# Optimization experiments

Measured on AMD Instinct MI355X. Metric: run time of the kernel, lower is better.

The kernel has to match this reference:

```python
import jax, jax.numpy as jnp
import numpy as np

T, H, F, E, K = 4096, 1024, 4096, 8, 2


def setup_inputs() -> dict:
    key = jax.random.key(0)
    ks = jax.random.split(key, 6)
    hidden_states = jax.random.normal(ks[0], (T, H), dtype=jnp.float32)
    expert_weights = jax.random.uniform(ks[1], (T, K), dtype=jnp.float32)
    selected_experts = jax.random.randint(ks[2], (T, K), 0, E, dtype=jnp.int64)
    W1 = 0.02 * jax.random.normal(ks[3], (E, H, F), dtype=jnp.float32)
    b1 = jnp.zeros((E, F), dtype=jnp.float32)
    W2 = 0.02 * jax.random.normal(ks[4], (E, F, H), dtype=jnp.float32)
    b2 = jnp.zeros((E, H), dtype=jnp.float32)
    return {"hidden_states": hidden_states, "expert_weights": expert_weights,
            "W1": W1, "b1": b1, "W2": W2, "b2": b2,
            "selected_experts": selected_experts}


def reference(hidden_states, expert_weights, W1, b1, W2, b2, selected_experts):
    # Combine weight per (token, expert): sum of routing weights over top-k
    # slots assigned to that expert; slots with expert_idx < 0 contribute 0.
    num_experts = W1.shape[0]
    onehot = (selected_experts[:, :, None] == jnp.arange(num_experts)[None, None, :])
    valid = (selected_experts >= 0)[:, :, None]
    cw = jnp.einsum('tk,tke->te', expert_weights,
                    (onehot & valid).astype(hidden_states.dtype))  # [T, E]

    out = jnp.zeros_like(hidden_states)
    for e in range(num_experts):  # small fixed expert count
        h = jax.nn.gelu(hidden_states @ W1[e] + b1[e], approximate=False)  # [T, F]
        y = h @ W2[e] + b2[e]                                              # [T, H]
        out = out + cw[:, e:e + 1] * y
    return out
```

## Files before the change

### kernel.cpp

```cpp
#include <hip/hip_runtime.h>
#include <hip/hip_bf16.h>

#define Td 4096
#define Hd 1024
#define Fd 4096
#define Ed 8
#define Rcap 8704

typedef __attribute__((ext_vector_type(8))) short bf16x8;
typedef __attribute__((ext_vector_type(4))) float f32x4;
typedef __attribute__((ext_vector_type(8))) unsigned short u16x8;

__device__ __forceinline__ unsigned short f32_to_bf16(float x) {
  unsigned int u = __float_as_uint(x);
  unsigned int r = (u + 0x7FFFu + ((u >> 16) & 1u)) >> 16;
  return (unsigned short)r;
}

__global__ __launch_bounds__(256) void cvt_bf16_kernel(const float* __restrict__ in,
                                                       unsigned short* __restrict__ outp, int n8) {
  int i = blockIdx.x * 256 + threadIdx.x;
  if (i >= n8) return;
  const float4* p = (const float4*)(in + (size_t)i * 8);
  float4 a = p[0], b = p[1];
  u16x8 o;
  o[0] = f32_to_bf16(a.x); o[1] = f32_to_bf16(a.y); o[2] = f32_to_bf16(a.z); o[3] = f32_to_bf16(a.w);
  o[4] = f32_to_bf16(b.x); o[5] = f32_to_bf16(b.y); o[6] = f32_to_bf16(b.z); o[7] = f32_to_bf16(b.w);
  *(u16x8*)(outp + (size_t)i * 8) = o;
}

__global__ __launch_bounds__(256) void transpose_cvt_kernel(const float* __restrict__ in,
                                                            unsigned short* __restrict__ outp,
                                                            int Rdm, int Cdm) {
  __shared__ float tile[64][68];
  int tilesR = Rdm >> 6, tilesC = Cdm >> 6;
  int per = tilesR * tilesC;
  int bid = blockIdx.x;
  int e = bid / per; int rem = bid - e * per;
  int tr = rem / tilesC; int tc = rem - tr * tilesC;
  int r0 = tr << 6, c0 = tc << 6;
  int tid = threadIdx.x;
  int rr = tid >> 2, cq = (tid & 3) << 4;
  const float* src = in + ((size_t)e * Rdm + r0 + rr) * Cdm + c0 + cq;
  float4 v0 = ((const float4*)src)[0];
  float4 v1 = ((const float4*)src)[1];
  float4 v2 = ((const float4*)src)[2];
  float4 v3 = ((const float4*)src)[3];
  *(float4*)&tile[rr][cq + 0]  = v0;
  *(float4*)&tile[rr][cq + 4]  = v1;
  *(float4*)&tile[rr][cq + 8]  = v2;
  *(float4*)&tile[rr][cq + 12] = v3;
  __syncthreads();
  u16x8 o0, o1;
#pragma unroll
  for (int j = 0; j < 8; j++) o0[j] = f32_to_bf16(tile[cq + j][rr]);
#pragma unroll
  for (int j = 0; j < 8; j++) o1[j] = f32_to_bf16(tile[cq + 8 + j][rr]);
  unsigned short* dst = outp + ((size_t)e * Cdm + c0 + rr) * Rdm + r0 + cq;
  *(u16x8*)dst = o0;
  *(u16x8*)(dst + 8) = o1;
}

__global__ void init_meta_kernel(int* cnt) {
  if (threadIdx.x < Ed) cnt[threadIdx.x] = 0;
}

__global__ __launch_bounds__(256) void route_kernel(const int* __restrict__ sel,
                                                    const float* __restrict__ ew,
                                                    int* cnt, int* idxT, float* wgtT) {
  int t = blockIdx.x * 256 + threadIdx.x;
  if (t >= Td) return;
  int e0 = sel[t * 2], e1 = sel[t * 2 + 1];
  float w0 = ew[t * 2], w1 = ew[t * 2 + 1];
  if (e0 == e1) { w0 += w1; e1 = -1; }
  if (e0 >= 0 && e0 < Ed) { int p = atomicAdd(&cnt[e0], 1); idxT[e0 * Td + p] = t; wgtT[e0 * Td + p] = w0; }
  if (e1 >= 0 && e1 < Ed) { int p = atomicAdd(&cnt[e1], 1); idxT[e1 * Td + p] = t; wgtT[e1 * Td + p] = w1; }
}

__global__ void scan_kernel(const int* cnt, int* off) {
  if (threadIdx.x == 0) {
    int acc = 0; off[0] = 0;
#pragma unroll
    for (int e = 0; e < Ed; e++) { acc += (cnt[e] + 63) & ~63; off[e + 1] = acc; }
  }
}

__global__ __launch_bounds__(256) void compact_kernel(const int* __restrict__ cnt,
                                                      const int* __restrict__ off,
                                                      const int* __restrict__ idxT,
                                                      const float* __restrict__ wgtT,
                                                      int* __restrict__ cidx,
                                                      float* __restrict__ cwgt) {
  int j = blockIdx.x * 256 + threadIdx.x;
  int e = j >> 12; int i = j & (Td - 1);
  int base = off[e], end = off[e + 1];
  int row = base + i;
  if (row < end) {
    if (i < cnt[e]) { cidx[row] = idxT[e * Td + i]; cwgt[row] = wgtT[e * Td + i]; }
    else            { cidx[row] = -1;               cwgt[row] = 0.f; }
  }
}

template <bool FIRST, int KD, int NC>
__global__ __launch_bounds__(256) void gemm_kernel(const unsigned short* __restrict__ Abase,
                                                   const unsigned short* __restrict__ Bt,
                                                   const float* __restrict__ bias,
                                                   const int* __restrict__ cidx,
                                                   const float* __restrict__ cwgt,
                                                   const int* __restrict__ off,
                                                   unsigned short* __restrict__ hbuf,
                                                   float* __restrict__ outp) {
  int row0 = blockIdx.y << 6;
  int tot = off[Ed];
  if (row0 >= tot) return;
  int e = 0;
  while (off[e + 1] <= row0) ++e;
  int n0 = blockIdx.x << 6;

  __shared__ unsigned short As[64][72];
  __shared__ unsigned short Bs[64][72];

  const int tid = threadIdx.x;
  const int sr = tid >> 2, sk = (tid & 3) << 4;

  bool avalid = true;
  const unsigned short* aptr;
  if (FIRST) {
    int t = cidx[row0 + sr];
    avalid = (t >= 0);
    aptr = Abase + (size_t)(avalid ? t : 0) * KD + sk;
  } else {
    aptr = Abase + (size_t)(row0 + sr) * KD + sk;
  }
  const unsigned short* bptr = Bt + ((size_t)e * NC + n0 + sr) * KD + sk;

  const int lane = tid & 63, wid = tid >> 6;
  const int wr = wid >> 1, wc = wid & 1;
  const int fr = lane & 15, fk = (lane >> 4) << 3;

  f32x4 acc[2][2] = {};

  for (int k0 = 0; k0 < KD; k0 += 64) {
    uint4 a0v = make_uint4(0, 0, 0, 0), a1v = a0v;
    if (avalid) {
      a0v = ((const uint4*)(aptr + k0))[0];
      a1v = ((const uint4*)(aptr + k0))[1];
    }
    uint4 b0v = ((const uint4*)(bptr + k0))[0];
    uint4 b1v = ((const uint4*)(bptr + k0))[1];
    __syncthreads();
    *(uint4*)(&As[sr][sk])     = a0v;
    *(uint4*)(&As[sr][sk + 8]) = a1v;
    *(uint4*)(&Bs[sr][sk])     = b0v;
    *(uint4*)(&Bs[sr][sk + 8]) = b1v;
    __syncthreads();
#pragma unroll
    for (int ks = 0; ks < 64; ks += 32) {
      bf16x8 af0 = *(const bf16x8*)(&As[(wr << 5) + fr][ks + fk]);
      bf16x8 af1 = *(const bf16x8*)(&As[(wr << 5) + 16 + fr][ks + fk]);
      bf16x8 bg0 = *(const bf16x8*)(&Bs[(wc << 5) + fr][ks + fk]);
      bf16x8 bg1 = *(const bf16x8*)(&Bs[(wc << 5) + 16 + fr][ks + fk]);
      acc[0][0] = __builtin_amdgcn_mfma_f32_16x16x32_bf16(af0, bg0, acc[0][0], 0, 0, 0);
      acc[0][1] = __builtin_amdgcn_mfma_f32_16x16x32_bf16(af0, bg1, acc[0][1], 0, 0, 0);
      acc[1][0] = __builtin_amdgcn_mfma_f32_16x16x32_bf16(af1, bg0, acc[1][0], 0, 0, 0);
      acc[1][1] = __builtin_amdgcn_mfma_f32_16x16x32_bf16(af1, bg1, acc[1][1], 0, 0, 0);
    }
  }

#pragma unroll
  for (int mi = 0; mi < 2; mi++) {
#pragma unroll
    for (int ni = 0; ni < 2; ni++) {
      int col = n0 + (wc << 5) + (ni << 4) + fr;
      float bval = bias[e * NC + col];
      f32x4 v = acc[mi][ni];
#pragma unroll
      for (int r2 = 0; r2 < 4; r2++) {
        int row = row0 + (wr << 5) + (mi << 4) + ((lane >> 4) << 2) + r2;
        float x = v[r2] + bval;
        if (FIRST) {
          float g = 0.5f * x * (1.0f + erff(x * 0.70710678118654752f));
          hbuf[(size_t)row * NC + col] = f32_to_bf16(g);
        } else {
          int tdst = cidx[row];
          if (tdst >= 0) {
            atomicAdd(outp + (size_t)tdst * NC + col, cwgt[row] * x);
          }
        }
      }
    }
  }
}

extern "C" void kernel_launch(void* const* d_in, const int* in_sizes, int n_in,
                              void* d_out, int out_size, void* d_ws, size_t ws_size,
                              hipStream_t stream) {
  const float* hidden = (const float*)d_in[0];
  const float* ew     = (const float*)d_in[1];
  const float* W1     = (const float*)d_in[2];
  const float* b1     = (const float*)d_in[3];
  const float* W2     = (const float*)d_in[4];
  const float* b2     = (const float*)d_in[5];
  const int*   sel    = (const int*)d_in[6];
  float* outp = (float*)d_out;

  unsigned short* hbf  = (unsigned short*)d_ws;
  unsigned short* W1T  = hbf + (size_t)Td * Hd;
  unsigned short* W2T  = W1T + (size_t)Ed * Fd * Hd;
  unsigned short* hbuf = W2T + (size_t)Ed * Hd * Fd;
  int*   cnt  = (int*)(hbuf + (size_t)Rcap * Fd);
  int*   off  = cnt + 16;
  int*   idxT = off + 16;
  float* wgtT = (float*)(idxT + Ed * Td);
  int*   cidx = (int*)(wgtT + Ed * Td);
  float* cwgt = (float*)(cidx + Rcap);

  (void)hipMemsetAsync(d_out, 0, (size_t)Td * Hd * sizeof(float), stream);

  cvt_bf16_kernel<<<(Td * Hd / 8 + 255) / 256, 256, 0, stream>>>(hidden, hbf, Td * Hd / 8);
  transpose_cvt_kernel<<<Ed * (Hd / 64) * (Fd / 64), 256, 0, stream>>>(W1, W1T, Hd, Fd);
  transpose_cvt_kernel<<<Ed * (Fd / 64) * (Hd / 64), 256, 0, stream>>>(W2, W2T, Fd, Hd);

  init_meta_kernel<<<1, 64, 0, stream>>>(cnt);
  route_kernel<<<Td / 256, 256, 0, stream>>>(sel, ew, cnt, idxT, wgtT);
  scan_kernel<<<1, 64, 0, stream>>>(cnt, off);
  compact_kernel<<<Ed * Td / 256, 256, 0, stream>>>(cnt, off, idxT, wgtT, cidx, cwgt);

  gemm_kernel<true, Hd, Fd><<<dim3(Fd / 64, Rcap / 64), 256, 0, stream>>>(
      hbf, W1T, b1, cidx, cwgt, off, hbuf, nullptr);
  gemm_kernel<false, Fd, Hd><<<dim3(Hd / 64, Rcap / 64), 256, 0, stream>>>(
      hbuf, W2T, b2, cidx, cwgt, off, nullptr, outp);
}
```

Measured before the change: 635.7 us.

## Enlarge MoE GEMM tiles and load operands directly into LDS

```diff
diff --git a/kernel.cpp b/kernel.cpp
--- a/kernel.cpp
+++ b/kernel.cpp
@@ -5,7 +5,7 @@
 #define Hd 1024
 #define Fd 4096
 #define Ed 8
-#define Rcap 8704
+#define Rcap 9216
 
 typedef __attribute__((ext_vector_type(8))) short bf16x8;
 typedef __attribute__((ext_vector_type(4))) float f32x4;
@@ -15,6 +15,12 @@
   unsigned int u = __float_as_uint(x);
   unsigned int r = (u + 0x7FFFu + ((u >> 16) & 1u)) >> 16;
   return (unsigned short)r;
+}
+
+__device__ __forceinline__ void gload_lds16(const unsigned short* g, unsigned short* l) {
+  __builtin_amdgcn_global_load_lds(
+      (const __attribute__((address_space(1))) unsigned int*)g,
+      (__attribute__((address_space(3))) unsigned int*)l, 16, 0, 0);
 }
 
 __global__ __launch_bounds__(256) void cvt_bf16_kernel(const float* __restrict__ in,
@@ -81,7 +87,7 @@
   if (threadIdx.x == 0) {
     int acc = 0; off[0] = 0;
 #pragma unroll
-    for (int e = 0; e < Ed; e++) { acc += (cnt[e] + 63) & ~63; off[e + 1] = acc; }
+    for (int e = 0; e < Ed; e++) { acc += (cnt[e] + 127) & ~127; off[e + 1] = acc; }
   }
 }
 
@@ -101,7 +107,7 @@
   }
 }
 
-template <bool FIRST, int KD, int NC>
+template <bool FIRST, int KD, int NC, int BN>
 __global__ __launch_bounds__(256) void gemm_kernel(const unsigned short* __restrict__ Abase,
                                                    const unsigned short* __restrict__ Bt,
                                                    const float* __restrict__ bias,
@@ -110,81 +116,91 @@
                                                    const int* __restrict__ off,
                                                    unsigned short* __restrict__ hbuf,
                                                    float* __restrict__ outp) {
-  int row0 = blockIdx.y << 6;
+  constexpr int NF = BN / 32;
+  int row0 = blockIdx.x << 7;
   int tot = off[Ed];
   if (row0 >= tot) return;
   int e = 0;
   while (off[e + 1] <= row0) ++e;
-  int n0 = blockIdx.x << 6;
-
-  __shared__ unsigned short As[64][72];
-  __shared__ unsigned short Bs[64][72];
+  int n0 = blockIdx.y * BN;
+
+  __shared__ unsigned short As[128][64];
+  __shared__ unsigned short Bs[BN][64];
 
   const int tid = threadIdx.x;
-  const int sr = tid >> 2, sk = (tid & 3) << 4;
-
-  bool avalid = true;
-  const unsigned short* aptr;
-  if (FIRST) {
-    int t = cidx[row0 + sr];
-    avalid = (t >= 0);
-    aptr = Abase + (size_t)(avalid ? t : 0) * KD + sk;
-  } else {
-    aptr = Abase + (size_t)(row0 + sr) * KD + sk;
-  }
-  const unsigned short* bptr = Bt + ((size_t)e * NC + n0 + sr) * KD + sk;
-
-  const int lane = tid & 63, wid = tid >> 6;
-  const int wr = wid >> 1, wc = wid & 1;
+  const int lane = tid & 63, w = tid >> 6;
+  const int wr = w >> 1, wc = w & 1;
   const int fr = lane & 15, fk = (lane >> 4) << 3;
 
-  f32x4 acc[2][2] = {};
+  const int sofs = (lane & 7) << 3;
+  const unsigned short* aptr[4];
+#pragma unroll
+  for (int i = 0; i < 4; i++) {
+    int ar = (w << 5) + (i << 3) + (lane >> 3);
+    int t;
+    if (FIRST) { t = cidx[row0 + ar]; if (t < 0) t = 0; }
+    else       { t = row0 + ar; }
+    aptr[i] = Abase + (size_t)t * KD + sofs;
+  }
+  const unsigned short* bptr[NF];
+#pragma unroll
+  for (int i = 0; i < NF; i++) {
+    int br = w * (BN / 4) + (i << 3) + (lane >> 3);
+    bptr[i] = Bt + ((size_t)e * NC + n0 + br) * KD + sofs;
+  }
+  unsigned short* alds = &As[0][0] + (w << 11);
+  unsigned short* blds = &Bs[0][0] + w * (BN * 16);
+
+  f32x4 acc[4][NF] = {};
 
   for (int k0 = 0; k0 < KD; k0 += 64) {
-    uint4 a0v = make_uint4(0, 0, 0, 0), a1v = a0v;
-    if (avalid) {
-      a0v = ((const uint4*)(aptr + k0))[0];
-      a1v = ((const uint4*)(aptr + k0))[1];
+    __syncthreads();
+#pragma unroll
+    for (int i = 0; i < 4; i++)  gload_lds16(aptr[i] + k0, alds + (i << 9));
+#pragma unroll
+    for (int i = 0; i < NF; i++) gload_lds16(bptr[i] + k0, blds + (i << 9));
+    __syncthreads();
+#pragma unroll
+    for (int ks = 0; ks < 64; ks += 32) {
+      bf16x8 af[4], bg[NF];
+#pragma unroll
+      for (int mi = 0; mi < 4; mi++)
+        af[mi] = *(const bf16x8*)&As[(wr << 6) + (mi << 4) + fr][ks + fk];
+#pragma unroll
+      for (int ni = 0; ni < NF; ni++)
+        bg[ni] = *(const bf16x8*)&Bs[wc * (BN / 2) + (ni << 4) + fr][ks + fk];
+#pragma unroll
+      for (int mi = 0; mi < 4; mi++)
+#pragma unroll
+        for (int ni = 0; ni < NF; ni++)
+          acc[mi][ni] = __builtin_amdgcn_mfma_f32_16x16x32_bf16(af[mi], bg[ni], acc[mi][ni], 0, 0, 0);
     }
-    uint4 b0v = ((const uint4*)(bptr + k0))[0];
-    uint4 b1v = ((const uint4*)(bptr + k0))[1];
-    __syncthreads();
-    *(uint4*)(&As[sr][sk])     = a0v;
-    *(uint4*)(&As[sr][sk + 8]) = a1v;
-    *(uint4*)(&Bs[sr][sk])     = b0v;
-    *(uint4*)(&Bs[sr][sk + 8]) = b1v;
-    __syncthreads();
-#pragma unroll
-    for (int ks = 0; ks < 64; ks += 32) {
-      bf16x8 af0 = *(const bf16x8*)(&As[(wr << 5) + fr][ks + fk]);
-      bf16x8 af1 = *(const bf16x8*)(&As[(wr << 5) + 16 + fr][ks + fk]);
-      bf16x8 bg0 = *(const bf16x8*)(&Bs[(wc << 5) + fr][ks + fk]);
-      bf16x8 bg1 = *(const bf16x8*)(&Bs[(wc << 5) + 16 + fr][ks + fk]);
-      acc[0][0] = __builtin_amdgcn_mfma_f32_16x16x32_bf16(af0, bg0, acc[0][0], 0, 0, 0);
-      acc[0][1] = __builtin_amdgcn_mfma_f32_16x16x32_bf16(af0, bg1, acc[0][1], 0, 0, 0);
-      acc[1][0] = __builtin_amdgcn_mfma_f32_16x16x32_bf16(af1, bg0, acc[1][0], 0, 0, 0);
-      acc[1][1] = __builtin_amdgcn_mfma_f32_16x16x32_bf16(af1, bg1, acc[1][1], 0, 0, 0);
-    }
-  }
-
-#pragma unroll
-  for (int mi = 0; mi < 2; mi++) {
-#pragma unroll
-    for (int ni = 0; ni < 2; ni++) {
-      int col = n0 + (wc << 5) + (ni << 4) + fr;
-      float bval = bias[e * NC + col];
-      f32x4 v = acc[mi][ni];
-#pragma unroll
-      for (int r2 = 0; r2 < 4; r2++) {
-        int row = row0 + (wr << 5) + (mi << 4) + ((lane >> 4) << 2) + r2;
-        float x = v[r2] + bval;
-        if (FIRST) {
+  }
+
+  float bv[NF];
+#pragma unroll
+  for (int ni = 0; ni < NF; ni++) bv[ni] = bias[e * NC + n0 + wc * (BN / 2) + (ni << 4) + fr];
+#pragma unroll
+  for (int mi = 0; mi < 4; mi++) {
+#pragma unroll
+    for (int r2 = 0; r2 < 4; r2++) {
+      int row = row0 + (wr << 6) + (mi << 4) + ((lane >> 4) << 2) + r2;
+      if (FIRST) {
+#pragma unroll
+        for (int ni = 0; ni < NF; ni++) {
+          int col = n0 + wc * (BN / 2) + (ni << 4) + fr;
+          float x = acc[mi][ni][r2] + bv[ni];
           float g = 0.5f * x * (1.0f + erff(x * 0.70710678118654752f));
           hbuf[(size_t)row * NC + col] = f32_to_bf16(g);
-        } else {
-          int tdst = cidx[row];
-          if (tdst >= 0) {
-            atomicAdd(outp + (size_t)tdst * NC + col, cwgt[row] * x);
+        }
+      } else {
+        int tdst = cidx[row];
+        float cw = cwgt[row];
+        if (tdst >= 0) {
+#pragma unroll
+          for (int ni = 0; ni < NF; ni++) {
+            int col = n0 + wc * (BN / 2) + (ni << 4) + fr;
+            atomicAdd(outp + (size_t)tdst * NC + col, cw * (acc[mi][ni][r2] + bv[ni]));
           }
         }
       }
@@ -226,8 +242,8 @@
   scan_kernel<<<1, 64, 0, stream>>>(cnt, off);
   compact_kernel<<<Ed * Td / 256, 256, 0, stream>>>(cnt, off, idxT, wgtT, cidx, cwgt);
 
-  gemm_kernel<true, Hd, Fd><<<dim3(Fd / 64, Rcap / 64), 256, 0, stream>>>(
+  gemm_kernel<true, Hd, Fd, 128><<<dim3(Rcap / 128, Fd / 128), 256, 0, stream>>>(
       hbf, W1T, b1, cidx, cwgt, off, hbuf, nullptr);
-  gemm_kernel<false, Fd, Hd><<<dim3(Hd / 64, Rcap / 64), 256, 0, stream>>>(
+  gemm_kernel<false, Fd, Hd, 64><<<dim3(Rcap / 128, Hd / 64), 256, 0, stream>>>(
       hbuf, W2T, b2, cidx, cwgt, off, nullptr, outp);
 }
```

After: 692.2 us. 1.09x slower.
